# Kernel tuning notes

Hardware: AMD Instinct MI355X
Metric: run time of the kernel (lower is better)

Reference implementation:

```python
import jax, jax.numpy as jnp
import numpy as np

U = 100000
I = 100000
N = U + I          # total nodes
D = 64             # emb_size
E = 2000000        # nnz of normalized adjacency
B = 4096           # lookup batch
N_LAYERS = 3
ALPHA = 0.1
BETA = 0.9


def _spmm(rows, cols, vals, x):
    # y = A @ x for COO sparse A: y[r] += v * x[c]
    return jax.ops.segment_sum(vals[:, None] * x[cols], rows, num_segments=N)


def setup_inputs() -> dict:
    key = jax.random.key(0)
    ks = jax.random.split(key, 7)
    users = jax.random.randint(ks[0], (B,), 0, U, dtype=jnp.int32)
    items = jax.random.randint(ks[1], (B,), 0, I, dtype=jnp.int32)
    # xavier-uniform-ish init
    lim = float(np.sqrt(6.0 / (U + D)))
    user_emb = jax.random.uniform(ks[2], (U, D), jnp.float32, -lim, lim)
    item_emb = jax.random.uniform(ks[3], (I, D), jnp.float32, -lim, lim)
    adj_rows = jax.random.randint(ks[4], (E,), 0, N, dtype=jnp.int32)
    adj_cols = jax.random.randint(ks[5], (E,), 0, N, dtype=jnp.int32)
    # normalized adjacency values are small positives ~ 1/sqrt(deg_i*deg_j)
    adj_vals = jax.random.uniform(ks[6], (E,), jnp.float32, 0.0, 0.2)
    return {"users": users, "items": items, "user_emb": user_emb,
            "item_emb": item_emb, "adj_rows": adj_rows,
            "adj_cols": adj_cols, "adj_vals": adj_vals}


def reference(users, items, user_emb, item_emb, adj_rows, adj_cols, adj_vals):
    gamma = BETA ** N_LAYERS + ALPHA * sum(BETA ** i for i in range(N_LAYERS))
    ego = jnp.concatenate([user_emb, item_emb], axis=0)  # [N, D]
    x0 = jnp.zeros_like(ego)
    for k in range(N_LAYERS):
        ego = _spmm(adj_rows, adj_cols, adj_vals, ego)
        if k == 0:
            x0 = ego
        else:
            ego = ego * BETA + x0 * ALPHA
    ego = ego / gamma
    user_e = ego[:U][users]   # [B, D]
    item_e = ego[U:][items]   # [B, D]
    return (user_e, item_e)
```

## Files before the change

### kernel.cpp

```cpp
#include <hip/hip_runtime.h>
#include <hip/hip_fp16.h>

#define D 64
#define BETA 0.9f
#define ALPHA 0.1f
#define CB_SHIFT 10
#define CB_ROWS 1024
#define CAP_SHIFT 14
#define CAP (1 << CAP_SHIFT)
#define SA_BLOCKS 128
#define CC_BLOCKS 256

typedef __attribute__((ext_vector_type(16))) int int16v;

__global__ void prep(const int* __restrict__ rows, const int* __restrict__ cols,
                     const float* __restrict__ vals, int E,
                     int* __restrict__ gcur, int2* __restrict__ tmp,
                     const float* __restrict__ u, const float* __restrict__ it,
                     long long UD, long long ND, __half* __restrict__ x,
                     int* __restrict__ flag2, int N) {
    __shared__ int hist[256];
    __shared__ int cur[256];
    int t = threadIdx.x;
    if (blockIdx.x < SA_BLOCKS) {
        if (t < 256) hist[t] = 0;
        __syncthreads();
        int chunk = (E + SA_BLOCKS - 1) / SA_BLOCKS;
        int beg = blockIdx.x * chunk;
        int end = min(beg + chunk, E);
        for (int e = beg + t; e < end; e += 1024)
            atomicAdd(&hist[rows[e] >> CB_SHIFT], 1);
        __syncthreads();
        if (t < 256) {
            int h = hist[t];
            cur[t] = h ? atomicAdd(&gcur[t], h) : 0;
        }
        __syncthreads();
        for (int e = beg + t; e < end; e += 1024) {
            int r = rows[e];
            int cb = r >> CB_SHIFT;
            int p = atomicAdd(&cur[cb], 1);
            tmp[((size_t)cb << CAP_SHIFT) + p] =
                make_int2(cols[e] | ((r & (CB_ROWS - 1)) << 18), __float_as_int(vals[e]));
        }
    } else {
        int lb = blockIdx.x - SA_BLOCKS;
        long long n4 = ND >> 2;
        long long stride = (long long)CC_BLOCKS * 1024;
        for (long long i4 = (long long)lb * 1024 + t; i4 < n4; i4 += stride) {
            long long base = i4 << 2;
            float4 v = (base < UD) ? ((const float4*)u)[i4]
                                   : ((const float4*)it)[(base - UD) >> 2];
            __half2* dst = (__half2*)(x + base);
            dst[0] = __floats2half2_rn(v.x, v.y);
            dst[1] = __floats2half2_rn(v.z, v.w);
        }
        for (long long i = (long long)lb * 1024 + t; i < N; i += stride)
            flag2[i] = 0;
    }
}

__global__ void stageB(const int* __restrict__ bcnt, int N,
                       const int2* __restrict__ tmp,
                       int2* __restrict__ epack, int2* __restrict__ meta) {
    __shared__ int sc[CB_ROWS];
    __shared__ int cur[CB_ROWS];
    int cb = blockIdx.x;
    int t = threadIdx.x;
    size_t base = (size_t)cb << CAP_SHIFT;
    int nb = bcnt[cb];
    sc[t] = 0;
    __syncthreads();
    for (int e = t; e < nb; e += CB_ROWS)
        atomicAdd(&sc[((unsigned)tmp[base + e].x) >> 18], 1);
    __syncthreads();
    int mycnt = sc[t];
    for (int off = 1; off < CB_ROWS; off <<= 1) {
        int v = (t >= off) ? sc[t - off] : 0;
        __syncthreads();
        sc[t] += v;
        __syncthreads();
    }
    int excl = sc[t] - mycnt;
    cur[t] = excl;
    int r = (cb << CB_SHIFT) + t;
    if (r < N) meta[r] = make_int2((int)base + excl, mycnt);
    __syncthreads();
    for (int e = t; e < nb; e += CB_ROWS) {
        int2 pk = tmp[base + e];
        int rl = ((unsigned)pk.x) >> 18;
        int p = atomicAdd(&cur[rl], 1);
        epack[base + p] = make_int2(pk.x & ((1 << 18) - 1), pk.y);
    }
}

__device__ __forceinline__ float row_dot_s(const int2* __restrict__ ep,
                                           int beg, int cnt,
                                           const __half* __restrict__ x, int lane) {
    float acc = 0.f;
    int e = 0;
    int full = cnt & ~15;
    for (; e < full; e += 16) {
        int16v ed0, ed1;
        asm volatile("s_load_dwordx16 %0, %2, 0x0\n\t"
                     "s_load_dwordx16 %1, %2, 0x40\n\t"
                     "s_waitcnt lgkmcnt(0)"
                     : "=s"(ed0), "=s"(ed1)
                     : "s"(ep + beg + e));
#define EDGEF(S, k)                                                           \
        acc += __int_as_float(S[2 * (k) + 1]) *                               \
               __half2float(x[((size_t)(unsigned)S[2 * (k)] << 6) + lane]);
        EDGEF(ed0, 0) EDGEF(ed0, 1) EDGEF(ed0, 2) EDGEF(ed0, 3)
        EDGEF(ed0, 4) EDGEF(ed0, 5) EDGEF(ed0, 6) EDGEF(ed0, 7)
        EDGEF(ed1, 0) EDGEF(ed1, 1) EDGEF(ed1, 2) EDGEF(ed1, 3)
        EDGEF(ed1, 4) EDGEF(ed1, 5) EDGEF(ed1, 6) EDGEF(ed1, 7)
#undef EDGEF
    }
    int rem = cnt - e;
    if (rem > 0) {
        int16v ed0, ed1;
        asm volatile("s_load_dwordx16 %0, %2, 0x0\n\t"
                     "s_load_dwordx16 %1, %2, 0x40\n\t"
                     "s_waitcnt lgkmcnt(0)"
                     : "=s"(ed0), "=s"(ed1)
                     : "s"(ep + beg + e));
#define EDGET(S, k, b)                                                        \
        {                                                                     \
            bool ok = ((b) + (k)) < rem;                                      \
            int col = ok ? S[2 * (k)] : 0;                                    \
            float v = ok ? __int_as_float(S[2 * (k) + 1]) : 0.0f;             \
            float xv = __half2float(x[((size_t)(unsigned)col << 6) + lane]);  \
            acc += ok ? v * xv : 0.0f;                                        \
        }
        EDGET(ed0, 0, 0) EDGET(ed0, 1, 0) EDGET(ed0, 2, 0) EDGET(ed0, 3, 0)
        EDGET(ed0, 4, 0) EDGET(ed0, 5, 0) EDGET(ed0, 6, 0) EDGET(ed0, 7, 0)
        EDGET(ed1, 0, 8) EDGET(ed1, 1, 8) EDGET(ed1, 2, 8) EDGET(ed1, 3, 8)
        EDGET(ed1, 4, 8) EDGET(ed1, 5, 8) EDGET(ed1, 6, 8) EDGET(ed1, 7, 8)
#undef EDGET
    }
    return acc;
}

__global__ void spmm_l0(const int2* __restrict__ meta, const int2* __restrict__ epack,
                        const __half* __restrict__ xcat, int N, __half* __restrict__ y,
                        __half* __restrict__ ego1_row0,
                        const int* __restrict__ users, const int* __restrict__ items,
                        int B, int U, int* __restrict__ flag2, int spmm_blocks) {
    int lane = threadIdx.x & 63;
    int wv = threadIdx.x >> 6;
    if (blockIdx.x >= spmm_blocks) {
        int w = (blockIdx.x - spmm_blocks) * 4 + wv;
        if (w >= 2 * B) return;
        int r = (w < B) ? users[w] : U + items[w - B];
        int2 m = meta[r];
        for (int e = m.x + lane; e < m.x + m.y; e += 64)
            flag2[epack[e].x] = 1;
        return;
    }
    if (blockIdx.x == 0 && threadIdx.x < D)
        ego1_row0[threadIdx.x] = __float2half(0.0f);
    int r = blockIdx.x * 4 + wv;
    if (r >= N) return;
    r = __builtin_amdgcn_readfirstlane(r);
    int2 m = meta[r];
    int beg = __builtin_amdgcn_readfirstlane(m.x);
    int cnt = __builtin_amdgcn_readfirstlane(m.y);
    float acc = row_dot_s(epack, beg, cnt, xcat, lane);
    y[((size_t)r << 6) + lane] = __float2half(acc);
}

__global__ void spmm_l1(const int2* __restrict__ meta, const int2* __restrict__ epack,
                        const __half* __restrict__ x0, const int* __restrict__ flag2,
                        int N, __half* __restrict__ y) {
    int lane = threadIdx.x & 63;
    int r = blockIdx.x * (blockDim.x >> 6) + (threadIdx.x >> 6);
    if (r >= N) return;
    r = __builtin_amdgcn_readfirstlane(r);
    if (flag2[r] == 0) return;
    int2 m = meta[r];
    int beg = __builtin_amdgcn_readfirstlane(m.x);
    int cnt = __builtin_amdgcn_readfirstlane(m.y);
    float acc = row_dot_s(epack, beg, cnt, x0, lane);
    float x0v = __half2float(x0[((size_t)r << 6) + lane]);
    y[((size_t)r << 6) + lane] = __float2half(BETA * acc + ALPHA * x0v);
}

__global__ void out_slots(const int* __restrict__ users, const int* __restrict__ items,
                          int B, int U,
                          const int2* __restrict__ meta, const int2* __restrict__ epack,
                          const __half* __restrict__ ego1, const __half* __restrict__ x0,
                          float inv_gamma, float* __restrict__ out) {
    int lane = threadIdx.x & 63;
    int w = blockIdx.x * (blockDim.x >> 6) + (threadIdx.x >> 6);
    if (w >= 2 * B) return;
    int r = (w < B) ? users[w] : U + items[w - B];
    r = __builtin_amdgcn_readfirstlane(r);
    int2 m = meta[r];
    int beg = __builtin_amdgcn_readfirstlane(m.x);
    int cnt = __builtin_amdgcn_readfirstlane(m.y);
    float acc = row_dot_s(epack, beg, cnt, ego1, lane);
    float x0v = __half2float(x0[((size_t)r << 6) + lane]);
    out[((size_t)w << 6) + lane] = (BETA * acc + ALPHA * x0v) * inv_gamma;
}

extern "C" void kernel_launch(void* const* d_in, const int* in_sizes, int n_in,
                              void* d_out, int out_size, void* d_ws, size_t ws_size,
                              hipStream_t stream) {
    const int*   users = (const int*)d_in[0];
    const int*   items = (const int*)d_in[1];
    const float* uemb  = (const float*)d_in[2];
    const float* iemb  = (const float*)d_in[3];
    const int*   arows = (const int*)d_in[4];
    const int*   acols = (const int*)d_in[5];
    const float* avals = (const float*)d_in[6];

    const int B = in_sizes[0];
    const int U = in_sizes[2] / D;
    const int I = in_sizes[3] / D;
    const int N = U + I;
    const int E = in_sizes[4];

    const double gamma_d = (double)BETA * BETA * BETA +
                           (double)ALPHA * (1.0 + (double)BETA + (double)BETA * BETA);
    const float inv_gamma = (float)(1.0 / gamma_d);

    const int NCB = (N + CB_ROWS - 1) / CB_ROWS;

    char* ws = (char*)d_ws;
    auto align256 = [](size_t x) { return (x + 255) & ~(size_t)255; };
    const size_t ndh_bytes = (size_t)N * D * sizeof(__half);
    const size_t cap_bytes = ((size_t)NCB << CAP_SHIFT) * sizeof(int2) + 128;
    __half* ego1   = (__half*)ws; ws += align256(ndh_bytes);
    int2*   tmp    = (int2*)ego1;
    __half* x0     = (__half*)ws; ws += align256(ndh_bytes);
    __half* xcat   = (__half*)ws; ws += align256(ndh_bytes);
    int2*  epack   = (int2*)ws;  ws += align256(cap_bytes);
    int2*  meta    = (int2*)ws;  ws += align256((size_t)N * sizeof(int2));
    int*   flag2   = (int*)ws;   ws += align256((size_t)N * sizeof(int));
    int*   gcur    = (int*)ws;   ws += align256(256 * sizeof(int));

    const int threads = 256;
    const int rows_per_block = threads / 64;
    const int spmm_grid = (N + rows_per_block - 1) / rows_per_block;
    const int slot_grid = (2 * B + rows_per_block - 1) / rows_per_block;

    hipMemsetAsync(gcur, 0, 256 * sizeof(int), stream);
    prep<<<SA_BLOCKS + CC_BLOCKS, 1024, 0, stream>>>(arows, acols, avals, E, gcur, tmp,
                                                     uemb, iemb, (long long)U * D,
                                                     (long long)N * D, xcat, flag2, N);
    stageB<<<NCB, CB_ROWS, 0, stream>>>(gcur, N, tmp, epack, meta);

    spmm_l0<<<spmm_grid + slot_grid, threads, 0, stream>>>(meta, epack, xcat, N, x0, ego1,
                                                           users, items, B, U, flag2,
                                                           spmm_grid);
    spmm_l1<<<spmm_grid, threads, 0, stream>>>(meta, epack, x0, flag2, N, ego1);
    out_slots<<<slot_grid, threads, 0, stream>>>(users, items, B, U, meta, epack,
                                                 ego1, x0, inv_gamma, (float*)d_out);
}
```

Measured before the change: 174.1 us.

## Process two rows per wavefront with interleaved gathers and split flag marking

Each wavefront now handles two rows at once in the SpMM layers and the output slots, loading 8 edges of each row per iteration and issuing the 16 gathers together to raise memory-level parallelism. The flag-marking work moves out of spmm_l0 into its own kernel launched beforehand. The cost is padding to the longer row of the pair, one extra launch, and a small increase in epack overread slack.

```diff
diff --git a/kernel.cpp b/kernel.cpp
--- a/kernel.cpp
+++ b/kernel.cpp
@@ -94,95 +94,101 @@
     }
 }
 
-__device__ __forceinline__ float row_dot_s(const int2* __restrict__ ep,
-                                           int beg, int cnt,
-                                           const __half* __restrict__ x, int lane) {
-    float acc = 0.f;
-    int e = 0;
-    int full = cnt & ~15;
-    for (; e < full; e += 16) {
-        int16v ed0, ed1;
+__device__ __forceinline__ void pair_dot(const int2* __restrict__ ep,
+                                         int begA, int cntA, int begB, int cntB,
+                                         const __half* __restrict__ x, int lane,
+                                         float& accA_o, float& accB_o) {
+    float accA = 0.f, accB = 0.f;
+    int mx = max(cntA, cntB);
+    for (int e = 0; e < mx; e += 8) {
+        int16v edA, edB;
         asm volatile("s_load_dwordx16 %0, %2, 0x0\n\t"
-                     "s_load_dwordx16 %1, %2, 0x40\n\t"
+                     "s_load_dwordx16 %1, %3, 0x0\n\t"
                      "s_waitcnt lgkmcnt(0)"
-                     : "=s"(ed0), "=s"(ed1)
-                     : "s"(ep + beg + e));
-#define EDGEF(S, k)                                                           \
-        acc += __int_as_float(S[2 * (k) + 1]) *                               \
-               __half2float(x[((size_t)(unsigned)S[2 * (k)] << 6) + lane]);
-        EDGEF(ed0, 0) EDGEF(ed0, 1) EDGEF(ed0, 2) EDGEF(ed0, 3)
-        EDGEF(ed0, 4) EDGEF(ed0, 5) EDGEF(ed0, 6) EDGEF(ed0, 7)
-        EDGEF(ed1, 0) EDGEF(ed1, 1) EDGEF(ed1, 2) EDGEF(ed1, 3)
-        EDGEF(ed1, 4) EDGEF(ed1, 5) EDGEF(ed1, 6) EDGEF(ed1, 7)
-#undef EDGEF
-    }
-    int rem = cnt - e;
-    if (rem > 0) {
-        int16v ed0, ed1;
-        asm volatile("s_load_dwordx16 %0, %2, 0x0\n\t"
-                     "s_load_dwordx16 %1, %2, 0x40\n\t"
-                     "s_waitcnt lgkmcnt(0)"
-                     : "=s"(ed0), "=s"(ed1)
-                     : "s"(ep + beg + e));
-#define EDGET(S, k, b)                                                        \
-        {                                                                     \
-            bool ok = ((b) + (k)) < rem;                                      \
-            int col = ok ? S[2 * (k)] : 0;                                    \
-            float v = ok ? __int_as_float(S[2 * (k) + 1]) : 0.0f;             \
-            float xv = __half2float(x[((size_t)(unsigned)col << 6) + lane]);  \
-            acc += ok ? v * xv : 0.0f;                                        \
-        }
-        EDGET(ed0, 0, 0) EDGET(ed0, 1, 0) EDGET(ed0, 2, 0) EDGET(ed0, 3, 0)
-        EDGET(ed0, 4, 0) EDGET(ed0, 5, 0) EDGET(ed0, 6, 0) EDGET(ed0, 7, 0)
-        EDGET(ed1, 0, 8) EDGET(ed1, 1, 8) EDGET(ed1, 2, 8) EDGET(ed1, 3, 8)
-        EDGET(ed1, 4, 8) EDGET(ed1, 5, 8) EDGET(ed1, 6, 8) EDGET(ed1, 7, 8)
-#undef EDGET
-    }
-    return acc;
+                     : "=s"(edA), "=s"(edB)
+                     : "s"(ep + begA + e), "s"(ep + begB + e));
+        int remA = cntA - e, remB = cntB - e;
+        float xa[8], xb[8];
+#pragma unroll
+        for (int k = 0; k < 8; ++k) {
+            int colA = (k < remA) ? edA[2 * k] : 0;
+            int colB = (k < remB) ? edB[2 * k] : 0;
+            xa[k] = __half2float(x[((size_t)(unsigned)colA << 6) + lane]);
+            xb[k] = __half2float(x[((size_t)(unsigned)colB << 6) + lane]);
+        }
+#pragma unroll
+        for (int k = 0; k < 8; ++k) {
+            accA += (k < remA) ? __int_as_float(edA[2 * k + 1]) * xa[k] : 0.f;
+            accB += (k < remB) ? __int_as_float(edB[2 * k + 1]) * xb[k] : 0.f;
+        }
+    }
+    accA_o = accA;
+    accB_o = accB;
 }
 
 __global__ void spmm_l0(const int2* __restrict__ meta, const int2* __restrict__ epack,
                         const __half* __restrict__ xcat, int N, __half* __restrict__ y,
-                        __half* __restrict__ ego1_row0,
-                        const int* __restrict__ users, const int* __restrict__ items,
-                        int B, int U, int* __restrict__ flag2, int spmm_blocks) {
-    int lane = threadIdx.x & 63;
-    int wv = threadIdx.x >> 6;
-    if (blockIdx.x >= spmm_blocks) {
-        int w = (blockIdx.x - spmm_blocks) * 4 + wv;
-        if (w >= 2 * B) return;
-        int r = (w < B) ? users[w] : U + items[w - B];
-        int2 m = meta[r];
-        for (int e = m.x + lane; e < m.x + m.y; e += 64)
-            flag2[epack[e].x] = 1;
-        return;
-    }
+                        __half* __restrict__ ego1_row0) {
+    int lane = threadIdx.x & 63;
     if (blockIdx.x == 0 && threadIdx.x < D)
         ego1_row0[threadIdx.x] = __float2half(0.0f);
-    int r = blockIdx.x * 4 + wv;
-    if (r >= N) return;
-    r = __builtin_amdgcn_readfirstlane(r);
+    int w = blockIdx.x * 4 + (threadIdx.x >> 6);
+    int rA = 2 * w;
+    if (rA >= N) return;
+    rA = __builtin_amdgcn_readfirstlane(rA);
+    int rB = rA + 1;
+    int2 mA = meta[rA];
+    int2 mB = meta[rB];
+    int begA = __builtin_amdgcn_readfirstlane(mA.x);
+    int cntA = __builtin_amdgcn_readfirstlane(mA.y);
+    int begB = __builtin_amdgcn_readfirstlane(mB.x);
+    int cntB = __builtin_amdgcn_readfirstlane(mB.y);
+    float accA, accB;
+    pair_dot(epack, begA, cntA, begB, cntB, xcat, lane, accA, accB);
+    y[((size_t)rA << 6) + lane] = __float2half(accA);
+    y[((size_t)rB << 6) + lane] = __float2half(accB);
+}
+
+__global__ void mark_flag2(const int* __restrict__ users, const int* __restrict__ items,
+                           int B, int U, const int2* __restrict__ meta,
+                           const int2* __restrict__ epack, int* __restrict__ flag2) {
+    int lane = threadIdx.x & 63;
+    int w = blockIdx.x * (blockDim.x >> 6) + (threadIdx.x >> 6);
+    if (w >= 2 * B) return;
+    int r = (w < B) ? users[w] : U + items[w - B];
     int2 m = meta[r];
-    int beg = __builtin_amdgcn_readfirstlane(m.x);
-    int cnt = __builtin_amdgcn_readfirstlane(m.y);
-    float acc = row_dot_s(epack, beg, cnt, xcat, lane);
-    y[((size_t)r << 6) + lane] = __float2half(acc);
+    for (int e = m.x + lane; e < m.x + m.y; e += 64)
+        flag2[epack[e].x] = 1;
 }
 
 __global__ void spmm_l1(const int2* __restrict__ meta, const int2* __restrict__ epack,
                         const __half* __restrict__ x0, const int* __restrict__ flag2,
                         int N, __half* __restrict__ y) {
     int lane = threadIdx.x & 63;
-    int r = blockIdx.x * (blockDim.x >> 6) + (threadIdx.x >> 6);
-    if (r >= N) return;
-    r = __builtin_amdgcn_readfirstlane(r);
-    if (flag2[r] == 0) return;
-    int2 m = meta[r];
-    int beg = __builtin_amdgcn_readfirstlane(m.x);
-    int cnt = __builtin_amdgcn_readfirstlane(m.y);
-    float acc = row_dot_s(epack, beg, cnt, x0, lane);
-    float x0v = __half2float(x0[((size_t)r << 6) + lane]);
-    y[((size_t)r << 6) + lane] = __float2half(BETA * acc + ALPHA * x0v);
+    int w = blockIdx.x * 4 + (threadIdx.x >> 6);
+    int rA = 2 * w;
+    if (rA >= N) return;
+    rA = __builtin_amdgcn_readfirstlane(rA);
+    int rB = rA + 1;
+    int fA = __builtin_amdgcn_readfirstlane(flag2[rA]);
+    int fB = __builtin_amdgcn_readfirstlane(flag2[rB]);
+    if (!(fA | fB)) return;
+    int2 mA = meta[rA];
+    int2 mB = meta[rB];
+    int begA = __builtin_amdgcn_readfirstlane(mA.x);
+    int cntA = fA ? __builtin_amdgcn_readfirstlane(mA.y) : 0;
+    int begB = __builtin_amdgcn_readfirstlane(mB.x);
+    int cntB = fB ? __builtin_amdgcn_readfirstlane(mB.y) : 0;
+    float accA, accB;
+    pair_dot(epack, begA, cntA, begB, cntB, x0, lane, accA, accB);
+    if (fA) {
+        float x0v = __half2float(x0[((size_t)rA << 6) + lane]);
+        y[((size_t)rA << 6) + lane] = __float2half(BETA * accA + ALPHA * x0v);
+    }
+    if (fB) {
+        float x0v = __half2float(x0[((size_t)rB << 6) + lane]);
+        y[((size_t)rB << 6) + lane] = __float2half(BETA * accB + ALPHA * x0v);
+    }
 }
 
 __global__ void out_slots(const int* __restrict__ users, const int* __restrict__ items,
@@ -191,16 +197,26 @@
                           const __half* __restrict__ ego1, const __half* __restrict__ x0,
                           float inv_gamma, float* __restrict__ out) {
     int lane = threadIdx.x & 63;
-    int w = blockIdx.x * (blockDim.x >> 6) + (threadIdx.x >> 6);
-    if (w >= 2 * B) return;
-    int r = (w < B) ? users[w] : U + items[w - B];
-    r = __builtin_amdgcn_readfirstlane(r);
-    int2 m = meta[r];
-    int beg = __builtin_amdgcn_readfirstlane(m.x);
-    int cnt = __builtin_amdgcn_readfirstlane(m.y);
-    float acc = row_dot_s(epack, beg, cnt, ego1, lane);
-    float x0v = __half2float(x0[((size_t)r << 6) + lane]);
-    out[((size_t)w << 6) + lane] = (BETA * acc + ALPHA * x0v) * inv_gamma;
+    int w = blockIdx.x * 4 + (threadIdx.x >> 6);
+    int sA = 2 * w;
+    if (sA >= 2 * B) return;
+    int sB = sA + 1;
+    int rA = (sA < B) ? users[sA] : U + items[sA - B];
+    int rB = (sB < B) ? users[sB] : U + items[sB - B];
+    rA = __builtin_amdgcn_readfirstlane(rA);
+    rB = __builtin_amdgcn_readfirstlane(rB);
+    int2 mA = meta[rA];
+    int2 mB = meta[rB];
+    int begA = __builtin_amdgcn_readfirstlane(mA.x);
+    int cntA = __builtin_amdgcn_readfirstlane(mA.y);
+    int begB = __builtin_amdgcn_readfirstlane(mB.x);
+    int cntB = __builtin_amdgcn_readfirstlane(mB.y);
+    float accA, accB;
+    pair_dot(epack, begA, cntA, begB, cntB, ego1, lane, accA, accB);
+    float xA = __half2float(x0[((size_t)rA << 6) + lane]);
+    float xB = __half2float(x0[((size_t)rB << 6) + lane]);
+    out[((size_t)sA << 6) + lane] = (BETA * accA + ALPHA * xA) * inv_gamma;
+    out[((size_t)sB << 6) + lane] = (BETA * accB + ALPHA * xB) * inv_gamma;
 }
 
 extern "C" void kernel_launch(void* const* d_in, const int* in_sizes, int n_in,
@@ -229,7 +245,7 @@
     char* ws = (char*)d_ws;
     auto align256 = [](size_t x) { return (x + 255) & ~(size_t)255; };
     const size_t ndh_bytes = (size_t)N * D * sizeof(__half);
-    const size_t cap_bytes = ((size_t)NCB << CAP_SHIFT) * sizeof(int2) + 128;
+    const size_t cap_bytes = ((size_t)NCB << CAP_SHIFT) * sizeof(int2) + 512;
     __half* ego1   = (__half*)ws; ws += align256(ndh_bytes);
     int2*   tmp    = (int2*)ego1;
     __half* x0     = (__half*)ws; ws += align256(ndh_bytes);
@@ -240,9 +256,9 @@
     int*   gcur    = (int*)ws;   ws += align256(256 * sizeof(int));
 
     const int threads = 256;
-    const int rows_per_block = threads / 64;
-    const int spmm_grid = (N + rows_per_block - 1) / rows_per_block;
-    const int slot_grid = (2 * B + rows_per_block - 1) / rows_per_block;
+    const int pair_grid = (N / 2 + 3) / 4;
+    const int slot_pair_grid = (2 * B / 2 + 3) / 4;
+    const int slot_grid = (2 * B + 3) / 4;
 
     hipMemsetAsync(gcur, 0, 256 * sizeof(int), stream);
     prep<<<SA_BLOCKS + CC_BLOCKS, 1024, 0, stream>>>(arows, acols, avals, E, gcur, tmp,
@@ -250,10 +266,9 @@
                                                      (long long)N * D, xcat, flag2, N);
     stageB<<<NCB, CB_ROWS, 0, stream>>>(gcur, N, tmp, epack, meta);
 
-    spmm_l0<<<spmm_grid + slot_grid, threads, 0, stream>>>(meta, epack, xcat, N, x0, ego1,
-                                                           users, items, B, U, flag2,
-                                                           spmm_grid);
-    spmm_l1<<<spmm_grid, threads, 0, stream>>>(meta, epack, x0, flag2, N, ego1);
-    out_slots<<<slot_grid, threads, 0, stream>>>(users, items, B, U, meta, epack,
-                                                 ego1, x0, inv_gamma, (float*)d_out);
-}
+    mark_flag2<<<slot_grid, threads, 0, stream>>>(users, items, B, U, meta, epack, flag2);
+    spmm_l0<<<pair_grid, threads, 0, stream>>>(meta, epack, xcat, N, x0, ego1);
+    spmm_l1<<<pair_grid, threads, 0, stream>>>(meta, epack, x0, flag2, N, ego1);
+    out_slots<<<slot_pair_grid, threads, 0, stream>>>(users, items, B, U, meta, epack,
+                                                      ego1, x0, inv_gamma, (float*)d_out);
+}
```

Result: slower. 184.7 us (+6.1%).

## Split each row's edges across four lane groups with 8-byte vector gathers

Applied to the files above, without the earlier changes.

The SpMM row kernels change from one lane per feature with scalar-loaded edge batches to four 16-lane groups. Each group handles a different edge and reads 4 halfs (8 bytes) per lane, and the groups are combined with xor shuffles at the end. The aim is to issue more independent gathers per wave and to use wider memory transactions on the fp16 embedding rows. The flag-marking work moves out of spmm_l0 into its own small kernel, which adds one launch. The extra shuffle reductions and the scatter of edge metadata across vector registers are the cost.

```diff
diff --git a/kernel.cpp b/kernel.cpp
--- a/kernel.cpp
+++ b/kernel.cpp
@@ -10,8 +10,6 @@
 #define CAP (1 << CAP_SHIFT)
 #define SA_BLOCKS 128
 #define CC_BLOCKS 256
-
-typedef __attribute__((ext_vector_type(16))) int int16v;
 
 __global__ void prep(const int* __restrict__ rows, const int* __restrict__ cols,
                      const float* __restrict__ vals, int E,
@@ -94,95 +92,115 @@
     }
 }
 
-__device__ __forceinline__ float row_dot_s(const int2* __restrict__ ep,
-                                           int beg, int cnt,
-                                           const __half* __restrict__ x, int lane) {
-    float acc = 0.f;
+__device__ __forceinline__ void row_accum(const int2* __restrict__ ep,
+                                          int beg, int cnt,
+                                          const __half* __restrict__ x,
+                                          int g, int foff,
+                                          float4& A0o, float4& A1o) {
+    const char* xb = (const char*)x;
+    float4 A0 = {0.f, 0.f, 0.f, 0.f}, A1 = {0.f, 0.f, 0.f, 0.f};
+    int full = cnt & ~7;
     int e = 0;
-    int full = cnt & ~15;
-    for (; e < full; e += 16) {
-        int16v ed0, ed1;
-        asm volatile("s_load_dwordx16 %0, %2, 0x0\n\t"
-                     "s_load_dwordx16 %1, %2, 0x40\n\t"
-                     "s_waitcnt lgkmcnt(0)"
-                     : "=s"(ed0), "=s"(ed1)
-                     : "s"(ep + beg + e));
-#define EDGEF(S, k)                                                           \
-        acc += __int_as_float(S[2 * (k) + 1]) *                               \
-               __half2float(x[((size_t)(unsigned)S[2 * (k)] << 6) + lane]);
-        EDGEF(ed0, 0) EDGEF(ed0, 1) EDGEF(ed0, 2) EDGEF(ed0, 3)
-        EDGEF(ed0, 4) EDGEF(ed0, 5) EDGEF(ed0, 6) EDGEF(ed0, 7)
-        EDGEF(ed1, 0) EDGEF(ed1, 1) EDGEF(ed1, 2) EDGEF(ed1, 3)
-        EDGEF(ed1, 4) EDGEF(ed1, 5) EDGEF(ed1, 6) EDGEF(ed1, 7)
-#undef EDGEF
+    for (; e < full; e += 8) {
+        int2 m0 = ep[beg + e + g];
+        int2 m1 = ep[beg + e + 4 + g];
+        uint2 q0 = *(const uint2*)(xb + (((size_t)(unsigned)m0.x) << 7) + foff);
+        uint2 q1 = *(const uint2*)(xb + (((size_t)(unsigned)m1.x) << 7) + foff);
+        float v0 = __int_as_float(m0.y), v1 = __int_as_float(m1.y);
+        float2 a = __half22float2(*(__half2*)&q0.x);
+        float2 b = __half22float2(*(__half2*)&q0.y);
+        float2 c = __half22float2(*(__half2*)&q1.x);
+        float2 d = __half22float2(*(__half2*)&q1.y);
+        A0.x += v0 * a.x; A0.y += v0 * a.y; A0.z += v0 * b.x; A0.w += v0 * b.y;
+        A1.x += v1 * c.x; A1.y += v1 * c.y; A1.z += v1 * d.x; A1.w += v1 * d.y;
     }
     int rem = cnt - e;
     if (rem > 0) {
-        int16v ed0, ed1;
-        asm volatile("s_load_dwordx16 %0, %2, 0x0\n\t"
-                     "s_load_dwordx16 %1, %2, 0x40\n\t"
-                     "s_waitcnt lgkmcnt(0)"
-                     : "=s"(ed0), "=s"(ed1)
-                     : "s"(ep + beg + e));
-#define EDGET(S, k, b)                                                        \
-        {                                                                     \
-            bool ok = ((b) + (k)) < rem;                                      \
-            int col = ok ? S[2 * (k)] : 0;                                    \
-            float v = ok ? __int_as_float(S[2 * (k) + 1]) : 0.0f;             \
-            float xv = __half2float(x[((size_t)(unsigned)col << 6) + lane]);  \
-            acc += ok ? v * xv : 0.0f;                                        \
-        }
-        EDGET(ed0, 0, 0) EDGET(ed0, 1, 0) EDGET(ed0, 2, 0) EDGET(ed0, 3, 0)
-        EDGET(ed0, 4, 0) EDGET(ed0, 5, 0) EDGET(ed0, 6, 0) EDGET(ed0, 7, 0)
-        EDGET(ed1, 0, 8) EDGET(ed1, 1, 8) EDGET(ed1, 2, 8) EDGET(ed1, 3, 8)
-        EDGET(ed1, 4, 8) EDGET(ed1, 5, 8) EDGET(ed1, 6, 8) EDGET(ed1, 7, 8)
-#undef EDGET
-    }
-    return acc;
+        int2 m0 = ep[beg + e + g];
+        int2 m1 = ep[beg + e + 4 + g];
+        bool ok0 = g < rem, ok1 = (g + 4) < rem;
+        int c0 = ok0 ? m0.x : 0;
+        int c1 = ok1 ? m1.x : 0;
+        float v0 = ok0 ? __int_as_float(m0.y) : 0.0f;
+        float v1 = ok1 ? __int_as_float(m1.y) : 0.0f;
+        uint2 q0 = *(const uint2*)(xb + (((size_t)(unsigned)c0) << 7) + foff);
+        uint2 q1 = *(const uint2*)(xb + (((size_t)(unsigned)c1) << 7) + foff);
+        float2 a = __half22float2(*(__half2*)&q0.x);
+        float2 b = __half22float2(*(__half2*)&q0.y);
+        float2 c = __half22float2(*(__half2*)&q1.x);
+        float2 d = __half22float2(*(__half2*)&q1.y);
+        A0.x += v0 * a.x; A0.y += v0 * a.y; A0.z += v0 * b.x; A0.w += v0 * b.y;
+        A1.x += v1 * c.x; A1.y += v1 * c.y; A1.z += v1 * d.x; A1.w += v1 * d.y;
+    }
+    A0o = A0; A1o = A1;
+}
+
+__device__ __forceinline__ float4 group_reduce(float4 A0, float4 A1) {
+    float4 A;
+    A.x = A0.x + A1.x; A.y = A0.y + A1.y; A.z = A0.z + A1.z; A.w = A0.w + A1.w;
+    A.x += __shfl_xor(A.x, 16); A.y += __shfl_xor(A.y, 16);
+    A.z += __shfl_xor(A.z, 16); A.w += __shfl_xor(A.w, 16);
+    A.x += __shfl_xor(A.x, 32); A.y += __shfl_xor(A.y, 32);
+    A.z += __shfl_xor(A.z, 32); A.w += __shfl_xor(A.w, 32);
+    return A;
 }
 
 __global__ void spmm_l0(const int2* __restrict__ meta, const int2* __restrict__ epack,
                         const __half* __restrict__ xcat, int N, __half* __restrict__ y,
-                        __half* __restrict__ ego1_row0,
-                        const int* __restrict__ users, const int* __restrict__ items,
-                        int B, int U, int* __restrict__ flag2, int spmm_blocks) {
-    int lane = threadIdx.x & 63;
-    int wv = threadIdx.x >> 6;
-    if (blockIdx.x >= spmm_blocks) {
-        int w = (blockIdx.x - spmm_blocks) * 4 + wv;
-        if (w >= 2 * B) return;
-        int r = (w < B) ? users[w] : U + items[w - B];
-        int2 m = meta[r];
-        for (int e = m.x + lane; e < m.x + m.y; e += 64)
-            flag2[epack[e].x] = 1;
-        return;
-    }
+                        __half* __restrict__ ego1_row0) {
     if (blockIdx.x == 0 && threadIdx.x < D)
         ego1_row0[threadIdx.x] = __float2half(0.0f);
-    int r = blockIdx.x * 4 + wv;
+    int lane = threadIdx.x & 63;
+    int g = lane >> 4, foff = (lane & 15) * 8;
+    int r = blockIdx.x * 4 + (threadIdx.x >> 6);
     if (r >= N) return;
-    r = __builtin_amdgcn_readfirstlane(r);
-    int2 m = meta[r];
-    int beg = __builtin_amdgcn_readfirstlane(m.x);
-    int cnt = __builtin_amdgcn_readfirstlane(m.y);
-    float acc = row_dot_s(epack, beg, cnt, xcat, lane);
-    y[((size_t)r << 6) + lane] = __float2half(acc);
+    int2 m = meta[r];
+    float4 A0, A1;
+    row_accum(epack, m.x, m.y, xcat, g, foff, A0, A1);
+    float4 A = group_reduce(A0, A1);
+    if (lane < 16) {
+        __half2 h0 = __floats2half2_rn(A.x, A.y);
+        __half2 h1 = __floats2half2_rn(A.z, A.w);
+        uint2 st = make_uint2(*(unsigned*)&h0, *(unsigned*)&h1);
+        *(uint2*)((char*)y + (((size_t)r) << 7) + foff) = st;
+    }
+}
+
+__global__ void mark_flag2(const int* __restrict__ users, const int* __restrict__ items,
+                           int B, int U, const int2* __restrict__ meta,
+                           const int2* __restrict__ epack, int* __restrict__ flag2) {
+    int lane = threadIdx.x & 63;
+    int w = blockIdx.x * (blockDim.x >> 6) + (threadIdx.x >> 6);
+    if (w >= 2 * B) return;
+    int r = (w < B) ? users[w] : U + items[w - B];
+    int2 m = meta[r];
+    for (int e = m.x + lane; e < m.x + m.y; e += 64)
+        flag2[epack[e].x] = 1;
 }
 
 __global__ void spmm_l1(const int2* __restrict__ meta, const int2* __restrict__ epack,
                         const __half* __restrict__ x0, const int* __restrict__ flag2,
                         int N, __half* __restrict__ y) {
     int lane = threadIdx.x & 63;
-    int r = blockIdx.x * (blockDim.x >> 6) + (threadIdx.x >> 6);
+    int g = lane >> 4, foff = (lane & 15) * 8;
+    int r = blockIdx.x * 4 + (threadIdx.x >> 6);
     if (r >= N) return;
-    r = __builtin_amdgcn_readfirstlane(r);
     if (flag2[r] == 0) return;
     int2 m = meta[r];
-    int beg = __builtin_amdgcn_readfirstlane(m.x);
-    int cnt = __builtin_amdgcn_readfirstlane(m.y);
-    float acc = row_dot_s(epack, beg, cnt, x0, lane);
-    float x0v = __half2float(x0[((size_t)r << 6) + lane]);
-    y[((size_t)r << 6) + lane] = __float2half(BETA * acc + ALPHA * x0v);
+    float4 A0, A1;
+    row_accum(epack, m.x, m.y, x0, g, foff, A0, A1);
+    float4 A = group_reduce(A0, A1);
+    if (lane < 16) {
+        uint2 xq = *(const uint2*)((const char*)x0 + (((size_t)r) << 7) + foff);
+        float2 xa = __half22float2(*(__half2*)&xq.x);
+        float2 xb = __half22float2(*(__half2*)&xq.y);
+        __half2 h0 = __floats2half2_rn(BETA * A.x + ALPHA * xa.x,
+                                       BETA * A.y + ALPHA * xa.y);
+        __half2 h1 = __floats2half2_rn(BETA * A.z + ALPHA * xb.x,
+                                       BETA * A.w + ALPHA * xb.y);
+        uint2 st = make_uint2(*(unsigned*)&h0, *(unsigned*)&h1);
+        *(uint2*)((char*)y + (((size_t)r) << 7) + foff) = st;
+    }
 }
 
 __global__ void out_slots(const int* __restrict__ users, const int* __restrict__ items,
@@ -191,16 +209,25 @@
                           const __half* __restrict__ ego1, const __half* __restrict__ x0,
                           float inv_gamma, float* __restrict__ out) {
     int lane = threadIdx.x & 63;
-    int w = blockIdx.x * (blockDim.x >> 6) + (threadIdx.x >> 6);
+    int g = lane >> 4, foff = (lane & 15) * 8;
+    int w = blockIdx.x * 4 + (threadIdx.x >> 6);
     if (w >= 2 * B) return;
     int r = (w < B) ? users[w] : U + items[w - B];
-    r = __builtin_amdgcn_readfirstlane(r);
-    int2 m = meta[r];
-    int beg = __builtin_amdgcn_readfirstlane(m.x);
-    int cnt = __builtin_amdgcn_readfirstlane(m.y);
-    float acc = row_dot_s(epack, beg, cnt, ego1, lane);
-    float x0v = __half2float(x0[((size_t)r << 6) + lane]);
-    out[((size_t)w << 6) + lane] = (BETA * acc + ALPHA * x0v) * inv_gamma;
+    int2 m = meta[r];
+    float4 A0, A1;
+    row_accum(epack, m.x, m.y, ego1, g, foff, A0, A1);
+    float4 A = group_reduce(A0, A1);
+    if (lane < 16) {
+        uint2 xq = *(const uint2*)((const char*)x0 + (((size_t)r) << 7) + foff);
+        float2 xa = __half22float2(*(__half2*)&xq.x);
+        float2 xb = __half22float2(*(__half2*)&xq.y);
+        float4 o;
+        o.x = (BETA * A.x + ALPHA * xa.x) * inv_gamma;
+        o.y = (BETA * A.y + ALPHA * xa.y) * inv_gamma;
+        o.z = (BETA * A.z + ALPHA * xb.x) * inv_gamma;
+        o.w = (BETA * A.w + ALPHA * xb.y) * inv_gamma;
+        *(float4*)((char*)out + (((size_t)w) << 8) + foff * 2) = o;
+    }
 }
 
 extern "C" void kernel_launch(void* const* d_in, const int* in_sizes, int n_in,
@@ -229,7 +256,7 @@
     char* ws = (char*)d_ws;
     auto align256 = [](size_t x) { return (x + 255) & ~(size_t)255; };
     const size_t ndh_bytes = (size_t)N * D * sizeof(__half);
-    const size_t cap_bytes = ((size_t)NCB << CAP_SHIFT) * sizeof(int2) + 128;
+    const size_t cap_bytes = ((size_t)NCB << CAP_SHIFT) * sizeof(int2) + 512;
     __half* ego1   = (__half*)ws; ws += align256(ndh_bytes);
     int2*   tmp    = (int2*)ego1;
     __half* x0     = (__half*)ws; ws += align256(ndh_bytes);
@@ -240,9 +267,8 @@
     int*   gcur    = (int*)ws;   ws += align256(256 * sizeof(int));
 
     const int threads = 256;
-    const int rows_per_block = threads / 64;
-    const int spmm_grid = (N + rows_per_block - 1) / rows_per_block;
-    const int slot_grid = (2 * B + rows_per_block - 1) / rows_per_block;
+    const int spmm_grid = (N + 3) / 4;
+    const int slot_grid = (2 * B + 3) / 4;
 
     hipMemsetAsync(gcur, 0, 256 * sizeof(int), stream);
     prep<<<SA_BLOCKS + CC_BLOCKS, 1024, 0, stream>>>(arows, acols, avals, E, gcur, tmp,
@@ -250,9 +276,8 @@
                                                      (long long)N * D, xcat, flag2, N);
     stageB<<<NCB, CB_ROWS, 0, stream>>>(gcur, N, tmp, epack, meta);
 
-    spmm_l0<<<spmm_grid + slot_grid, threads, 0, stream>>>(meta, epack, xcat, N, x0, ego1,
-                                                           users, items, B, U, flag2,
-                                                           spmm_grid);
+    mark_flag2<<<slot_grid, threads, 0, stream>>>(users, items, B, U, meta, epack, flag2);
+    spmm_l0<<<spmm_grid, threads, 0, stream>>>(meta, epack, xcat, N, x0, ego1);
     spmm_l1<<<spmm_grid, threads, 0, stream>>>(meta, epack, x0, flag2, N, ego1);
     out_slots<<<slot_grid, threads, 0, stream>>>(users, items, B, U, meta, epack,
                                                  ego1, x0, inv_gamma, (float*)d_out);
```

After: 177.7 us. 2.1% more time.
